# Optimization experiments

Hardware: AMD Instinct MI355X
Metric: run time of the kernel (lower is better)

The kernel has to match this reference:

```python
import jax, jax.numpy as jnp
import numpy as np

B, N, D = 32, 16384, 64        # batch, num inputs (128*128 feature map), slot dim
NS, ITERS, H = 7, 3, 128       # num slots, routing iters, mlp hidden (max(dim,128))
EPS = 1e-8
SCALE = D ** -0.5


def ln(x, g, b):
    # LayerNorm over last dim, eps=1e-5 (matches nn.LayerNorm defaults used)
    m = jnp.mean(x, axis=-1, keepdims=True)
    v = jnp.mean((x - m) ** 2, axis=-1, keepdims=True)
    return (x - m) * jax.lax.rsqrt(v + 1e-5) * g + b


def setup_inputs() -> dict:
    key = jax.random.key(0)
    ks = jax.random.split(key, 24)
    w = lambda k, shape, s=0.02: jax.random.normal(k, shape, dtype=jnp.float32) * s
    inp = {
        "inputs": jax.random.normal(ks[0], (B, N, D), dtype=jnp.float32),
        "noise": jax.random.normal(ks[1], (B, NS, D), dtype=jnp.float32),
        "slots_mu": w(ks[2], (1, 1, D), 1.0),
        "slots_sigma": jnp.abs(w(ks[3], (1, 1, D), 1.0)),  # used directly as std, as in torch.normal(mu, sigma)
        "Wq": w(ks[4], (D, D)), "bq": jnp.zeros((D,), jnp.float32),
        "Wk": w(ks[5], (D, D)), "bk": jnp.zeros((D,), jnp.float32),
        "Wv": w(ks[6], (D, D)), "bv": jnp.zeros((D,), jnp.float32),
        "W_ih": w(ks[7], (3 * D, D)), "W_hh": w(ks[8], (3 * D, D)),
        "b_ih": jnp.zeros((3 * D,), jnp.float32), "b_hh": jnp.zeros((3 * D,), jnp.float32),
        "mW1": w(ks[9], (H, D)), "mb1": jnp.zeros((H,), jnp.float32),
        "mW2": w(ks[10], (D, H)), "mb2": jnp.zeros((D,), jnp.float32),
        "g_in": jnp.ones((D,), jnp.float32), "b_in": jnp.zeros((D,), jnp.float32),
        "g_sl": jnp.ones((D,), jnp.float32), "b_sl": jnp.zeros((D,), jnp.float32),
        "g_ml": jnp.ones((D,), jnp.float32), "b_ml": jnp.zeros((D,), jnp.float32),
    }
    return inp


def reference(inputs, noise, slots_mu, slots_sigma, Wq, bq, Wk, bk, Wv, bv,
              W_ih, W_hh, b_ih, b_hh, mW1, mb1, mW2, mb2,
              g_in, b_in, g_sl, b_sl, g_ml, b_ml):
    # slots ~ Normal(mu, sigma): mu + sigma * eps
    slots = slots_mu + slots_sigma * noise                      # [B, NS, D]
    x = ln(inputs, g_in, b_in)                                  # [B, N, D]
    k = x @ Wk.T + bk                                           # [B, N, D]
    v = x @ Wv.T + bv                                           # [B, N, D]

    for _ in range(ITERS):
        slots_prev = slots
        s = ln(slots, g_sl, b_sl)
        q = s @ Wq.T + bq                                       # [B, NS, D]
        dots = jnp.einsum('bid,bjd->bij', q, k) * SCALE         # [B, NS, N]
        attn = jax.nn.softmax(dots, axis=1) + EPS               # softmax over SLOTS
        attn = attn / jnp.sum(attn, axis=-1, keepdims=True)     # renorm over keys
        updates = jnp.einsum('bjd,bij->bid', v, attn)           # [B, NS, D]
        # GRUCell(updates, slots_prev) over flattened (B*NS, D)
        xg = updates.reshape(-1, D) @ W_ih.T + b_ih             # [B*NS, 3D]
        hg = slots_prev.reshape(-1, D) @ W_hh.T + b_hh
        ir, iz, in_ = jnp.split(xg, 3, axis=-1)
        hr, hz, hn = jnp.split(hg, 3, axis=-1)
        r = jax.nn.sigmoid(ir + hr)
        z = jax.nn.sigmoid(iz + hz)
        n = jnp.tanh(in_ + r * hn)
        h = slots_prev.reshape(-1, D)
        slots = ((1.0 - z) * n + z * h).reshape(B, NS, D)
        # residual MLP
        m = ln(slots, g_ml, b_ml)
        slots = slots + (jax.nn.relu(m @ mW1.T + mb1) @ mW2.T + mb2)
    return slots
```

## Files before the change

### kernel.cpp

```cpp
#include <hip/hip_runtime.h>
#include <hip/hip_bf16.h>

typedef unsigned short u16;
typedef __bf16 bf16x8 __attribute__((ext_vector_type(8)));
typedef float  f32x4  __attribute__((ext_vector_type(4)));

#define N_  16384
#define SCALE_ 0.125f
#define TILE 128
#define TPAD 66
#define APAD 264

__device__ __forceinline__ u16 f2b(float f){
  unsigned u = __float_as_uint(f);
  unsigned r = (u + 0x7fffu + ((u>>16)&1u)) >> 16;
  return (u16)r;
}
__device__ __forceinline__ float blo(unsigned u){ return __uint_as_float(u<<16); }
__device__ __forceinline__ float bhi(unsigned u){ return __uint_as_float(u & 0xffff0000u); }
__device__ __forceinline__ float b2f(u16 v){ return __uint_as_float(((unsigned)v)<<16); }
__device__ __forceinline__ void ld8(const float* __restrict__ p, float* f){
  const float4 a = ((const float4*)p)[0];
  const float4 b = ((const float4*)p)[1];
  f[0]=a.x; f[1]=a.y; f[2]=a.z; f[3]=a.w;
  f[4]=b.x; f[5]=b.y; f[6]=b.z; f[7]=b.w;
}
__device__ __forceinline__ bf16x8 frag8(const float* __restrict__ p){
  float f[8]; ld8(p, f);
  bf16x8 r;
  #pragma unroll
  for (int j=0;j<8;++j) r[j] = (__bf16)f[j];
  return r;
}
__device__ __forceinline__ void unpk4u(uint4 u, float* f){
  f[0]=blo(u.x); f[1]=bhi(u.x);
  f[2]=blo(u.y); f[3]=bhi(u.y);
  f[4]=blo(u.z); f[5]=bhi(u.z);
  f[6]=blo(u.w); f[7]=bhi(u.w);
}

__global__ __launch_bounds__(256) void k_marker(float* __restrict__ out, int n, float val){
  const int i = blockIdx.x*256 + threadIdx.x;
  if (i < n) out[i] = val;
}

__global__ __launch_bounds__(256) void k_init_slots(
  const float* __restrict__ mu, const float* __restrict__ sigma,
  const float* __restrict__ noise, float* __restrict__ slots)
{
  const int idx = blockIdx.x*256 + threadIdx.x;
  const int d = idx & 63;
  slots[idx] = mu[d] + sigma[d] * noise[idx];
}

__global__ __launch_bounds__(256) void k_wkt(const float* __restrict__ Wk, float* __restrict__ wkT){
  const int i = blockIdx.x*256 + threadIdx.x;
  const int e = i>>6, d = i&63;
  wkT[i] = Wk[d*64 + e];
}

__global__ __launch_bounds__(256) void k_xln(
  const float* __restrict__ x, const float* __restrict__ g_in, const float* __restrict__ b_in,
  u16* __restrict__ xout)
{
  const int t = threadIdx.x;
  const long blk = blockIdx.x;
  const float4 gv = *(const float4*)(g_in + (t&15)*4);
  const float4 bb = *(const float4*)(b_in + (t&15)*4);
  const float* xbase = x + blk*16384;
  u16* obase = xout + blk*16384;
  float4 v[16];
  #pragma unroll
  for (int p=0;p<16;++p) v[p] = *(const float4*)(xbase + p*1024 + t*4);
  #pragma unroll
  for (int p=0;p<16;++p){
    float s = v[p].x + v[p].y + v[p].z + v[p].w;
    float q = v[p].x*v[p].x + v[p].y*v[p].y + v[p].z*v[p].z + v[p].w*v[p].w;
    #pragma unroll
    for (int off=1; off<16; off<<=1){ s += __shfl_xor(s, off); q += __shfl_xor(q, off); }
    const float mean = s*(1.f/64.f);
    const float rstd = rsqrtf(q*(1.f/64.f) - mean*mean + 1e-5f);
    const u16 e0 = f2b((v[p].x-mean)*rstd*gv.x + bb.x);
    const u16 e1 = f2b((v[p].y-mean)*rstd*gv.y + bb.y);
    const u16 e2 = f2b((v[p].z-mean)*rstd*gv.z + bb.z);
    const u16 e3 = f2b((v[p].w-mean)*rstd*gv.w + bb.w);
    const unsigned w0 = (unsigned)e0 | ((unsigned)e1<<16);
    const unsigned w1 = (unsigned)e2 | ((unsigned)e3<<16);
    *(uint2*)(obase + p*1024 + t*4) = make_uint2(w0, w1);
  }
}

__global__ __launch_bounds__(256) void k_qln_zero(
  const float* __restrict__ slots, const float* __restrict__ Wq, const float* __restrict__ bq,
  const float* __restrict__ g_sl, const float* __restrict__ b_sl,
  const float* __restrict__ wkT, const float* __restrict__ bk,
  float* __restrict__ qout, float* __restrict__ qkb, float* __restrict__ qbb,
  float* __restrict__ num, float* __restrict__ den, const int do_qk)
{
  const int tid = blockIdx.x*256 + threadIdx.x;
  num[tid] = 0.f;
  if (tid < 224) den[tid] = 0.f;
  const int ri = tid >> 6, lane = tid & 63;
  const float xv = slots[ri*64 + lane];
  float s = xv, ss = xv*xv;
  #pragma unroll
  for (int off=1; off<64; off<<=1){ s += __shfl_xor(s,off); ss += __shfl_xor(ss,off); }
  const float mean = s*(1.f/64.f);
  const float rstd = rsqrtf(ss*(1.f/64.f) - mean*mean + 1e-5f);
  const float sn = (xv-mean)*rstd*g_sl[lane] + b_sl[lane];
  float acc = 0.f;
  for (int d8=0; d8<8; ++d8){
    float wf[8]; ld8(Wq + lane*64 + d8*8, wf);
    #pragma unroll
    for (int j=0;j<8;++j) acc += __shfl(sn, d8*8+j) * wf[j];
  }
  const float qv = acc + bq[lane];
  qout[ri*64+lane] = qv;
  if (do_qk){
    float pb = qv * bk[lane];
    #pragma unroll
    for (int off=1; off<64; off<<=1) pb += __shfl_xor(pb, off);
    if (lane == 0) qbb[ri] = pb;
    float qkv = 0.f;
    for (int d8=0; d8<8; ++d8){
      float wf[8]; ld8(wkT + lane*64 + d8*8, wf);
      #pragma unroll
      for (int j=0;j<8;++j) qkv += __shfl(qv, d8*8+j) * wf[j];
    }
    qkb[ri*64+lane] = qkv;
  }
}

__global__ __launch_bounds__(256) void k_attn3(
  const u16* __restrict__ xln, const float* __restrict__ qkb, const float* __restrict__ qbb,
  float* __restrict__ num, float* __restrict__ den)
{
  __shared__ __align__(16) u16   xs[256*64];
  __shared__ __align__(16) u16   atb[7*APAD];
  __shared__ __align__(16) float qs[448];
  __shared__ float qbs[7];
  __shared__ float den_s[7];
  const int t = threadIdx.x;
  const int b = blockIdx.x >> 5, ch = blockIdx.x & 31;
  for (int i=t;i<448;i+=256) qs[i] = qkb[b*448+i];
  if (t<7){ qbs[t] = qbb[b*7+t]; den_s[t] = 0.f; }
  const int wid = t>>6, lane = t&63;
  const u16* gbase = xln + ((long)b*N_ + ch*512)*64;
  uint4 st[8];
  f32x4 accv = {0.f,0.f,0.f,0.f};

  #pragma unroll
  for (int p=0;p<8;++p) st[p] = *(const uint4*)(gbase + p*2048 + t*8);
  #pragma unroll
  for (int p=0;p<8;++p)
    *(uint4*)&xs[(p*32 + (t>>3))*64 + (((t&7) ^ ((t>>3)&7))<<3)] = st[p];
  __syncthreads();
  #pragma unroll
  for (int p=0;p<8;++p) st[p] = *(const uint4*)(gbase + 16384 + p*2048 + t*8);

  auto phaseA = [&](){
    float acc[7];
    #pragma unroll
    for (int i=0;i<7;++i) acc[i]=0.f;
    #pragma unroll
    for (int seg=0; seg<8; ++seg){
      const uint4 kw = *(const uint4*)&xs[t*64 + ((seg ^ (t&7))<<3)];
      float kf[8]; unpk4u(kw, kf);
      #pragma unroll
      for (int i=0;i<7;++i){
        const float4 qa = *(const float4*)&qs[i*64 + seg*8];
        const float4 qb4 = *(const float4*)&qs[i*64 + seg*8 + 4];
        acc[i] += kf[0]*qa.x + kf[1]*qa.y + kf[2]*qa.z + kf[3]*qa.w
                + kf[4]*qb4.x + kf[5]*qb4.y + kf[6]*qb4.z + kf[7]*qb4.w;
      }
    }
    float mx = -1e30f;
    #pragma unroll
    for (int i=0;i<7;++i){ acc[i] = (acc[i] + qbs[i]) * SCALE_; mx = fmaxf(mx, acc[i]); }
    float e[7]; float sum = 0.f;
    #pragma unroll
    for (int i=0;i<7;++i){ e[i] = __expf(acc[i]-mx); sum += e[i]; }
    const float inv = 1.f/sum;
    float dsum[7];
    #pragma unroll
    for (int i=0;i<7;++i){
      const u16 rb = f2b(e[i]*inv + 1e-8f);
      atb[i*APAD + t] = rb;
      dsum[i] = b2f(rb);
    }
    #pragma unroll
    for (int i=0;i<7;++i){
      #pragma unroll
      for (int off=1; off<64; off<<=1) dsum[i] += __shfl_xor(dsum[i], off);
    }
    if (lane == 0){
      #pragma unroll
      for (int i=0;i<7;++i) atomicAdd(&den_s[i], dsum[i]);
    }
  };

  const int m15 = lane & 15;
  const int kq = (lane>>4)<<3;
  const int dim2 = ((wid<<4) + m15) << 1;
  auto phaseB = [&](){
    #pragma unroll
    for (int ks=0; ks<8; ++ks){
      const int kbase = ks*32 + kq;
      const unsigned a0 = xs[(kbase+0)*64 + ((dim2 ^ (0<<4))>>1)];
      const unsigned a1 = xs[(kbase+1)*64 + ((dim2 ^ (1<<4))>>1)];
      const unsigned a2 = xs[(kbase+2)*64 + ((dim2 ^ (2<<4))>>1)];
      const unsigned a3 = xs[(kbase+3)*64 + ((dim2 ^ (3<<4))>>1)];
      const unsigned a4 = xs[(kbase+4)*64 + ((dim2 ^ (4<<4))>>1)];
      const unsigned a5 = xs[(kbase+5)*64 + ((dim2 ^ (5<<4))>>1)];
      const unsigned a6 = xs[(kbase+6)*64 + ((dim2 ^ (6<<4))>>1)];
      const unsigned a7 = xs[(kbase+7)*64 + ((dim2 ^ (7<<4))>>1)];
      const uint4 aw = make_uint4(a0|(a1<<16), a2|(a3<<16), a4|(a5<<16), a6|(a7<<16));
      const bf16x8 af = __builtin_bit_cast(bf16x8, aw);
      uint4 bw = make_uint4(0u,0u,0u,0u);
      if (m15 < 7) bw = *(const uint4*)&atb[m15*APAD + kbase];
      const bf16x8 bfv = __builtin_bit_cast(bf16x8, bw);
      accv = __builtin_amdgcn_mfma_f32_16x16x32_bf16(af, bfv, accv, 0,0,0);
    }
  };

  phaseA();
  __syncthreads();
  phaseB();
  __syncthreads();
  #pragma unroll
  for (int p=0;p<8;++p)
    *(uint4*)&xs[(p*32 + (t>>3))*64 + (((t&7) ^ ((t>>3)&7))<<3)] = st[p];
  __syncthreads();
  phaseA();
  __syncthreads();
  if (t < 7) atomicAdd(&den[b*7+t], den_s[t]);
  phaseB();

  if (m15 < 7){
    float* np = &num[((long)b*7 + m15)*64 + (wid<<4) + ((lane>>4)<<2)];
    #pragma unroll
    for (int r=0;r<4;++r) atomicAdd(np + r, accv[r]);
  }
}

__global__ __launch_bounds__(256) void k_attn_fused(
  const float* __restrict__ x,
  const float* __restrict__ Wk, const float* __restrict__ bk,
  const float* __restrict__ Wv, const float* __restrict__ bv,
  const float* __restrict__ g_in, const float* __restrict__ b_in,
  const float* __restrict__ qbuf, float* __restrict__ num, float* __restrict__ den)
{
  __shared__ __align__(16) u16   tile[TILE*TPAD];
  __shared__ __align__(16) float qs[7*64];
  __shared__ __align__(16) float at[7*TILE];
  const int t = threadIdx.x;
  const int b = blockIdx.x >> 6, ch = blockIdx.x & 63;
  for (int i=t; i<448; i+=256) qs[i] = qbuf[b*448 + i];
  const int wid = t>>6, lane = t&63;
  const int m = lane & 15, q4 = lane >> 4;
  float gf[16], bfv[16];
  ld8(g_in + q4*8, gf);  ld8(g_in + 32 + q4*8, gf+8);
  ld8(b_in + q4*8, bfv); ld8(b_in + 32 + q4*8, bfv+8);
  const int i0 = wid*2, i1 = wid*2+1;
  float n0=0.f, n1=0.f, d0=0.f, d1=0.f;

  for (int tl=0; tl<2; ++tl){
    const long j0 = (long)ch*256 + tl*TILE;
    const long rowbase = (long)b*N_ + j0 + (long)wid*32;
    __syncthreads();
    bf16x8 af[2][2];
    #pragma unroll
    for (int rg=0; rg<2; ++rg){
      const float* xr = x + (rowbase + rg*16 + m)*64;
      float xf[16];
      ld8(xr + q4*8, xf); ld8(xr + 32 + q4*8, xf+8);
      float s=0.f, ss=0.f;
      #pragma unroll
      for (int i=0;i<16;++i){ s += xf[i]; ss += xf[i]*xf[i]; }
      s  += __shfl_xor(s,16);  s  += __shfl_xor(s,32);
      ss += __shfl_xor(ss,16); ss += __shfl_xor(ss,32);
      const float mean = s*(1.f/64.f);
      const float rstd = rsqrtf(ss*(1.f/64.f) - mean*mean + 1e-5f);
      #pragma unroll
      for (int j=0;j<8;++j){
        af[rg][0][j] = (__bf16)((xf[j]  -mean)*rstd*gf[j]   + bfv[j]);
        af[rg][1][j] = (__bf16)((xf[8+j]-mean)*rstd*gf[8+j] + bfv[8+j]);
      }
    }
    {
      bf16x8 w0[4], w1[4]; float bc[4];
      #pragma unroll
      for (int cg=0; cg<4; ++cg){
        const int n = cg*16 + m;
        w0[cg] = frag8(Wk + n*64 + q4*8);
        w1[cg] = frag8(Wk + n*64 + 32 + q4*8);
        bc[cg] = bk[n];
      }
      #pragma unroll
      for (int rg=0; rg<2; ++rg){
        #pragma unroll
        for (int cg=0; cg<4; ++cg){
          f32x4 acc = {0.f,0.f,0.f,0.f};
          acc = __builtin_amdgcn_mfma_f32_16x16x32_bf16(af[rg][0], w0[cg], acc, 0,0,0);
          acc = __builtin_amdgcn_mfma_f32_16x16x32_bf16(af[rg][1], w1[cg], acc, 0,0,0);
          const int col = cg*16 + m;
          #pragma unroll
          for (int r=0;r<4;++r)
            tile[(wid*32 + rg*16 + q4*4 + r)*TPAD + col] = f2b(acc[r] + bc[cg]);
        }
      }
    }
    __syncthreads();
    if (t < TILE){
      float acc[7];
      #pragma unroll
      for (int i=0;i<7;++i) acc[i]=0.f;
      const unsigned* krow = (const unsigned*)&tile[t*TPAD];
      for (int wq=0; wq<8; ++wq){
        const unsigned k0 = krow[wq*4+0], k1 = krow[wq*4+1], k2 = krow[wq*4+2], k3 = krow[wq*4+3];
        float kf[8];
        kf[0]=blo(k0); kf[1]=bhi(k0); kf[2]=blo(k1); kf[3]=bhi(k1);
        kf[4]=blo(k2); kf[5]=bhi(k2); kf[6]=blo(k3); kf[7]=bhi(k3);
        #pragma unroll
        for (int i=0;i<7;++i){
          const float4 qa = *(const float4*)&qs[i*64 + wq*8];
          const float4 qb = *(const float4*)&qs[i*64 + wq*8 + 4];
          acc[i] += kf[0]*qa.x + kf[1]*qa.y + kf[2]*qa.z + kf[3]*qa.w
                  + kf[4]*qb.x + kf[5]*qb.y + kf[6]*qb.z + kf[7]*qb.w;
        }
      }
      float mx = -1e30f;
      #pragma unroll
      for (int i=0;i<7;++i){ acc[i] *= SCALE_; mx = fmaxf(mx, acc[i]); }
      float e[7]; float sum = 0.f;
      #pragma unroll
      for (int i=0;i<7;++i){ e[i] = __expf(acc[i]-mx); sum += e[i]; }
      const float inv = 1.f/sum;
      #pragma unroll
      for (int i=0;i<7;++i) at[i*TILE + t] = e[i]*inv + 1e-8f;
    }
    __syncthreads();
    {
      bf16x8 w0[4], w1[4]; float bc[4];
      #pragma unroll
      for (int cg=0; cg<4; ++cg){
        const int n = cg*16 + m;
        w0[cg] = frag8(Wv + n*64 + q4*8);
        w1[cg] = frag8(Wv + n*64 + 32 + q4*8);
        bc[cg] = bv[n];
      }
      #pragma unroll
      for (int rg=0; rg<2; ++rg){
        #pragma unroll
        for (int cg=0; cg<4; ++cg){
          f32x4 acc = {0.f,0.f,0.f,0.f};
          acc = __builtin_amdgcn_mfma_f32_16x16x32_bf16(af[rg][0], w0[cg], acc, 0,0,0);
          acc = __builtin_amdgcn_mfma_f32_16x16x32_bf16(af[rg][1], w1[cg], acc, 0,0,0);
          const int col = cg*16 + m;
          #pragma unroll
          for (int r=0;r<4;++r)
            tile[(wid*32 + rg*16 + q4*4 + r)*TPAD + col] = f2b(acc[r] + bc[cg]);
        }
      }
    }
    __syncthreads();
    #pragma unroll 4
    for (int j=0;j<TILE;++j){
      const unsigned vw = ((const unsigned*)&tile[j*TPAD])[lane>>1];
      const float vf = (lane&1) ? bhi(vw) : blo(vw);
      const float a0v = at[i0*TILE+j];
      n0 += a0v*vf; d0 += a0v;
      if (i1 < 7){ const float a1v = at[i1*TILE+j]; n1 += a1v*vf; d1 += a1v; }
    }
  }
  atomicAdd(&num[(b*7+i0)*64 + lane], n0);
  if (lane==0) atomicAdd(&den[b*7+i0], d0);
  if (i1 < 7){
    atomicAdd(&num[(b*7+i1)*64 + lane], n1);
    if (lane==0) atomicAdd(&den[b*7+i1], d1);
  }
}

__global__ __launch_bounds__(256) void k_gru_mlp(
  const float* __restrict__ num, const float* __restrict__ den, float* __restrict__ slots,
  const float* __restrict__ Wv, const float* __restrict__ bv,
  const float* __restrict__ Wih, const float* __restrict__ Whh,
  const float* __restrict__ bih, const float* __restrict__ bhh,
  const float* __restrict__ mW1, const float* __restrict__ mb1,
  const float* __restrict__ mW2, const float* __restrict__ mb2,
  const float* __restrict__ g_ml, const float* __restrict__ b_ml,
  float* __restrict__ outp, const int write_out, const int fastmode)
{
  const int tid = blockIdx.x*256 + threadIdx.x;
  const int ri = tid>>6, lane = tid&63;
  const float dn = den[ri];
  const float a = (dn > 0.f) ? (num[ri*64+lane] / dn) : 0.f;
  float u;
  if (fastmode){
    float acc = 0.f;
    for (int e8=0; e8<8; ++e8){
      float f[8]; ld8(Wv + lane*64 + e8*8, f);
      #pragma unroll
      for (int j=0;j<8;++j) acc += __shfl(a, e8*8+j) * f[j];
    }
    u = acc + bv[lane];
  } else {
    u = a;
  }
  const float h = slots[ri*64+lane];
  float air=0,aiz=0,ain=0,ahr=0,ahz=0,ahn=0;
  for (int d8=0; d8<8; ++d8){
    float fir[8],fiz[8],fin[8],fhr[8],fhz[8],fhn[8];
    ld8(Wih + (      lane)*64 + d8*8, fir);
    ld8(Wih + ( 64 + lane)*64 + d8*8, fiz);
    ld8(Wih + (128 + lane)*64 + d8*8, fin);
    ld8(Whh + (      lane)*64 + d8*8, fhr);
    ld8(Whh + ( 64 + lane)*64 + d8*8, fhz);
    ld8(Whh + (128 + lane)*64 + d8*8, fhn);
    #pragma unroll
    for (int j=0;j<8;++j){
      const float ud = __shfl(u, d8*8+j);
      const float hd = __shfl(h, d8*8+j);
      air += ud*fir[j]; aiz += ud*fiz[j]; ain += ud*fin[j];
      ahr += hd*fhr[j]; ahz += hd*fhz[j]; ahn += hd*fhn[j];
    }
  }
  air += bih[lane]; aiz += bih[64+lane]; ain += bih[128+lane];
  ahr += bhh[lane]; ahz += bhh[64+lane]; ahn += bhh[128+lane];
  const float r = 1.f/(1.f + __expf(-(air+ahr)));
  const float z = 1.f/(1.f + __expf(-(aiz+ahz)));
  const float n = tanhf(ain + r*ahn);
  const float sv = (1.f-z)*n + z*h;
  float s=sv, ss=sv*sv;
  #pragma unroll
  for (int off=1; off<64; off<<=1){ s += __shfl_xor(s,off); ss += __shfl_xor(ss,off); }
  const float mean = s*(1.f/64.f);
  const float rstd = rsqrtf(ss*(1.f/64.f) - mean*mean + 1e-5f);
  const float m = (sv-mean)*rstd*g_ml[lane] + b_ml[lane];
  float h1a=0.f, h1b=0.f;
  for (int d8=0; d8<8; ++d8){
    float f1[8], f2[8];
    ld8(mW1 + (     lane)*64 + d8*8, f1);
    ld8(mW1 + (64 + lane)*64 + d8*8, f2);
    #pragma unroll
    for (int j=0;j<8;++j){
      const float md = __shfl(m, d8*8+j);
      h1a += md*f1[j]; h1b += md*f2[j];
    }
  }
  h1a = fmaxf(h1a + mb1[lane], 0.f);
  h1b = fmaxf(h1b + mb1[64+lane], 0.f);
  float o = 0.f;
  for (int h8=0; h8<8; ++h8){
    float fa[8], fb[8];
    ld8(mW2 + lane*128 + h8*8, fa);
    ld8(mW2 + lane*128 + 64 + h8*8, fb);
    #pragma unroll
    for (int j=0;j<8;++j){
      o += __shfl(h1a, h8*8+j)*fa[j] + __shfl(h1b, h8*8+j)*fb[j];
    }
  }
  o += mb2[lane];
  const float res = sv + o;
  slots[ri*64+lane] = res;
  if (write_out) outp[ri*64+lane] = res;
}

extern "C" void kernel_launch(void* const* d_in, const int* in_sizes, int n_in,
                              void* d_out, int out_size, void* d_ws, size_t ws_size,
                              hipStream_t stream)
{
  float* outp = (float*)d_out;
  static const int EXP[24] = {33554432,14336,64,64, 4096,64, 4096,64, 4096,64,
                              12288,12288,192,192, 8192,128, 8192,64,
                              64,64, 64,64, 64,64};
  if (n_in != 24){ k_marker<<<56,256,0,stream>>>(outp, out_size, 30.f); return; }
  for (int i=0;i<24;++i)
    if (in_sizes[i] != EXP[i]){ k_marker<<<56,256,0,stream>>>(outp, out_size, 40.f+(float)i); return; }
  if (out_size != 14336){ k_marker<<<56,256,0,stream>>>(outp, out_size, 33.f); return; }
  if (ws_size < 200000){ k_marker<<<56,256,0,stream>>>(outp, out_size, 35.f); return; }

  const float* inputs = (const float*)d_in[0];
  const float* noise  = (const float*)d_in[1];
  const float* mu     = (const float*)d_in[2];
  const float* sigma  = (const float*)d_in[3];
  const float* Wq  = (const float*)d_in[4];  const float* bq  = (const float*)d_in[5];
  const float* Wk  = (const float*)d_in[6];  const float* bk  = (const float*)d_in[7];
  const float* Wv  = (const float*)d_in[8];  const float* bv  = (const float*)d_in[9];
  const float* Wih = (const float*)d_in[10]; const float* Whh = (const float*)d_in[11];
  const float* bih = (const float*)d_in[12]; const float* bhh = (const float*)d_in[13];
  const float* mW1 = (const float*)d_in[14]; const float* mb1 = (const float*)d_in[15];
  const float* mW2 = (const float*)d_in[16]; const float* mb2 = (const float*)d_in[17];
  const float* g_in = (const float*)d_in[18]; const float* b_in = (const float*)d_in[19];
  const float* g_sl = (const float*)d_in[20]; const float* b_sl = (const float*)d_in[21];
  const float* g_ml = (const float*)d_in[22]; const float* b_ml = (const float*)d_in[23];

  char* ws = (char*)d_ws;
  float* slots = (float*)ws;
  float* qbuf  = (float*)(ws + 57344);
  float* qkb   = (float*)(ws + 114688);
  float* num   = (float*)(ws + 172032);
  float* den   = (float*)(ws + 229376);
  float* qbb   = (float*)(ws + 230272);
  float* wkT   = (float*)(ws + 231168);
  u16* xln     = (u16*)(ws + 247808);
  const bool fast = (ws_size >= (size_t)247808 + 67108864ull);

  k_init_slots<<<56,256,0,stream>>>(mu, sigma, noise, slots);
  if (fast){
    k_wkt<<<16,256,0,stream>>>(Wk, wkT);
    k_xln<<<2048,256,0,stream>>>(inputs, g_in, b_in, xln);
  }
  for (int it=0; it<3; ++it){
    k_qln_zero<<<56,256,0,stream>>>(slots, Wq, bq, g_sl, b_sl, wkT, bk,
                                    qbuf, qkb, qbb, num, den, fast ? 1 : 0);
    if (fast)
      k_attn3<<<1024,256,0,stream>>>(xln, qkb, qbb, num, den);
    else
      k_attn_fused<<<2048,256,0,stream>>>(inputs, Wk, bk, Wv, bv, g_in, b_in, qbuf, num, den);
    k_gru_mlp<<<56,256,0,stream>>>(num, den, slots, Wv, bv, Wih, Whh, bih, bhh,
                                   mW1, mb1, mW2, mb2, g_ml, b_ml,
                                   outp, it==2 ? 1 : 0, fast ? 1 : 0);
  }
}
```

Measured before the change: 452.8 us.

## Use MFMA for slot-key dots, shrink attention tiles, fuse q projection into GRU kernel

The attention kernel now computes the q·k logits with bf16 MFMA instructions instead of scalar FMAs. It processes 128 keys per block across 4096 blocks, replacing 512-key blocks that double-buffered through registers. The q/LayerNorm projection and the num/den zeroing move into the init and GRU/MLP kernels, which removes one launch per iteration. In exchange, q is rounded to bf16 and there are more global atomics on den and num, since the block-local den reduction is gone and there are four times as many blocks.

```diff
diff --git a/kernel.cpp b/kernel.cpp
--- a/kernel.cpp
+++ b/kernel.cpp
@@ -9,7 +9,7 @@
 #define SCALE_ 0.125f
 #define TILE 128
 #define TPAD 66
-#define APAD 264
+#define AP4 136
 
 __device__ __forceinline__ u16 f2b(float f){
   unsigned u = __float_as_uint(f);
@@ -32,25 +32,65 @@
   for (int j=0;j<8;++j) r[j] = (__bf16)f[j];
   return r;
 }
-__device__ __forceinline__ void unpk4u(uint4 u, float* f){
-  f[0]=blo(u.x); f[1]=bhi(u.x);
-  f[2]=blo(u.y); f[3]=bhi(u.y);
-  f[4]=blo(u.z); f[5]=bhi(u.z);
-  f[6]=blo(u.w); f[7]=bhi(u.w);
-}
 
 __global__ __launch_bounds__(256) void k_marker(float* __restrict__ out, int n, float val){
   const int i = blockIdx.x*256 + threadIdx.x;
   if (i < n) out[i] = val;
 }
 
-__global__ __launch_bounds__(256) void k_init_slots(
+__device__ __forceinline__ void q_from_slots(
+  const float sv, const int ri, const int lane,
+  const float* __restrict__ Wq, const float* __restrict__ bq,
+  const float* __restrict__ g_sl, const float* __restrict__ b_sl,
+  const float* __restrict__ wkT, const float* __restrict__ bk,
+  float* __restrict__ qout, float* __restrict__ qkb, float* __restrict__ qbb,
+  const int do_qk)
+{
+  float s = sv, ss = sv*sv;
+  #pragma unroll
+  for (int off=1; off<64; off<<=1){ s += __shfl_xor(s,off); ss += __shfl_xor(ss,off); }
+  const float mean = s*(1.f/64.f);
+  const float rstd = rsqrtf(ss*(1.f/64.f) - mean*mean + 1e-5f);
+  const float sn = (sv-mean)*rstd*g_sl[lane] + b_sl[lane];
+  float acc = 0.f;
+  for (int d8=0; d8<8; ++d8){
+    float wf[8]; ld8(Wq + lane*64 + d8*8, wf);
+    #pragma unroll
+    for (int j=0;j<8;++j) acc += __shfl(sn, d8*8+j) * wf[j];
+  }
+  const float qv = acc + bq[lane];
+  qout[ri*64+lane] = qv;
+  if (do_qk){
+    float pb = qv * bk[lane];
+    #pragma unroll
+    for (int off=1; off<64; off<<=1) pb += __shfl_xor(pb, off);
+    if (lane == 0) qbb[ri] = pb;
+    float qkv = 0.f;
+    for (int d8=0; d8<8; ++d8){
+      float wf[8]; ld8(wkT + lane*64 + d8*8, wf);
+      #pragma unroll
+      for (int j=0;j<8;++j) qkv += __shfl(qv, d8*8+j) * wf[j];
+    }
+    qkb[ri*64+lane] = qkv;
+  }
+}
+
+__global__ __launch_bounds__(256) void k_init_slots_q(
   const float* __restrict__ mu, const float* __restrict__ sigma,
-  const float* __restrict__ noise, float* __restrict__ slots)
-{
-  const int idx = blockIdx.x*256 + threadIdx.x;
-  const int d = idx & 63;
-  slots[idx] = mu[d] + sigma[d] * noise[idx];
+  const float* __restrict__ noise, float* __restrict__ slots,
+  const float* __restrict__ Wq, const float* __restrict__ bq,
+  const float* __restrict__ g_sl, const float* __restrict__ b_sl,
+  const float* __restrict__ wkT, const float* __restrict__ bk,
+  float* __restrict__ qout, float* __restrict__ qkb, float* __restrict__ qbb,
+  float* __restrict__ num, float* __restrict__ den, const int do_qk)
+{
+  const int tid = blockIdx.x*256 + threadIdx.x;
+  const int ri = tid>>6, lane = tid&63;
+  const float sv = mu[lane] + sigma[lane] * noise[tid];
+  slots[tid] = sv;
+  num[tid] = 0.f;
+  if (tid < 224) den[tid] = 0.f;
+  q_from_slots(sv, ri, lane, Wq, bq, g_sl, b_sl, wkT, bk, qout, qkb, qbb, do_qk);
 }
 
 __global__ __launch_bounds__(256) void k_wkt(const float* __restrict__ Wk, float* __restrict__ wkT){
@@ -90,93 +130,67 @@
   }
 }
 
-__global__ __launch_bounds__(256) void k_qln_zero(
-  const float* __restrict__ slots, const float* __restrict__ Wq, const float* __restrict__ bq,
-  const float* __restrict__ g_sl, const float* __restrict__ b_sl,
-  const float* __restrict__ wkT, const float* __restrict__ bk,
-  float* __restrict__ qout, float* __restrict__ qkb, float* __restrict__ qbb,
-  float* __restrict__ num, float* __restrict__ den, const int do_qk)
-{
-  const int tid = blockIdx.x*256 + threadIdx.x;
-  num[tid] = 0.f;
-  if (tid < 224) den[tid] = 0.f;
-  const int ri = tid >> 6, lane = tid & 63;
-  const float xv = slots[ri*64 + lane];
-  float s = xv, ss = xv*xv;
-  #pragma unroll
-  for (int off=1; off<64; off<<=1){ s += __shfl_xor(s,off); ss += __shfl_xor(ss,off); }
-  const float mean = s*(1.f/64.f);
-  const float rstd = rsqrtf(ss*(1.f/64.f) - mean*mean + 1e-5f);
-  const float sn = (xv-mean)*rstd*g_sl[lane] + b_sl[lane];
-  float acc = 0.f;
-  for (int d8=0; d8<8; ++d8){
-    float wf[8]; ld8(Wq + lane*64 + d8*8, wf);
-    #pragma unroll
-    for (int j=0;j<8;++j) acc += __shfl(sn, d8*8+j) * wf[j];
-  }
-  const float qv = acc + bq[lane];
-  qout[ri*64+lane] = qv;
-  if (do_qk){
-    float pb = qv * bk[lane];
-    #pragma unroll
-    for (int off=1; off<64; off<<=1) pb += __shfl_xor(pb, off);
-    if (lane == 0) qbb[ri] = pb;
-    float qkv = 0.f;
-    for (int d8=0; d8<8; ++d8){
-      float wf[8]; ld8(wkT + lane*64 + d8*8, wf);
-      #pragma unroll
-      for (int j=0;j<8;++j) qkv += __shfl(qv, d8*8+j) * wf[j];
-    }
-    qkb[ri*64+lane] = qkv;
-  }
-}
-
-__global__ __launch_bounds__(256) void k_attn3(
+__global__ __launch_bounds__(256) void k_attn4(
   const u16* __restrict__ xln, const float* __restrict__ qkb, const float* __restrict__ qbb,
   float* __restrict__ num, float* __restrict__ den)
 {
-  __shared__ __align__(16) u16   xs[256*64];
-  __shared__ __align__(16) u16   atb[7*APAD];
-  __shared__ __align__(16) float qs[448];
+  __shared__ __align__(16) u16   xs[128*64];
+  __shared__ __align__(16) u16   atb[7*AP4];
+  __shared__ __align__(16) float dlds[128*9];
   __shared__ float qbs[7];
-  __shared__ float den_s[7];
   const int t = threadIdx.x;
-  const int b = blockIdx.x >> 5, ch = blockIdx.x & 31;
-  for (int i=t;i<448;i+=256) qs[i] = qkb[b*448+i];
-  if (t<7){ qbs[t] = qbb[b*7+t]; den_s[t] = 0.f; }
+  const int b = blockIdx.x >> 7, ch = blockIdx.x & 127;
   const int wid = t>>6, lane = t&63;
-  const u16* gbase = xln + ((long)b*N_ + ch*512)*64;
-  uint4 st[8];
-  f32x4 accv = {0.f,0.f,0.f,0.f};
-
-  #pragma unroll
-  for (int p=0;p<8;++p) st[p] = *(const uint4*)(gbase + p*2048 + t*8);
-  #pragma unroll
-  for (int p=0;p<8;++p)
+  const int m15 = lane&15, g4 = lane>>4;
+
+  const u16* gbase = xln + ((long)b*N_ + ch*128)*64;
+  uint4 st[4];
+  #pragma unroll
+  for (int p=0;p<4;++p) st[p] = *(const uint4*)(gbase + p*2048 + t*8);
+  if (t < 7) qbs[t] = qbb[b*7+t];
+  bf16x8 qf[2];
+  #pragma unroll
+  for (int f=0; f<2; ++f){
+    float tmp[8];
+    if (m15 < 7){ ld8(qkb + b*448 + m15*64 + f*32 + g4*8, tmp); }
+    else {
+      #pragma unroll
+      for (int j=0;j<8;++j) tmp[j]=0.f;
+    }
+    #pragma unroll
+    for (int j=0;j<8;++j) qf[f][j] = (__bf16)tmp[j];
+  }
+  #pragma unroll
+  for (int p=0;p<4;++p)
     *(uint4*)&xs[(p*32 + (t>>3))*64 + (((t&7) ^ ((t>>3)&7))<<3)] = st[p];
   __syncthreads();
-  #pragma unroll
-  for (int p=0;p<8;++p) st[p] = *(const uint4*)(gbase + 16384 + p*2048 + t*8);
-
-  auto phaseA = [&](){
+
+  #pragma unroll
+  for (int mt=0; mt<2; ++mt){
+    const int kr = (wid<<5) + (mt<<4) + m15;
+    f32x4 dacc = {0.f,0.f,0.f,0.f};
+    #pragma unroll
+    for (int f=0; f<2; ++f){
+      const int c = (f<<2) + g4;
+      const uint4 aw = *(const uint4*)&xs[kr*64 + ((c ^ (kr&7))<<3)];
+      dacc = __builtin_amdgcn_mfma_f32_16x16x32_bf16(
+               __builtin_bit_cast(bf16x8, aw), qf[f], dacc, 0,0,0);
+    }
+    if (m15 < 7){
+      const int krow = (wid<<5) + (mt<<4) + (g4<<2);
+      #pragma unroll
+      for (int r=0;r<4;++r) dlds[(krow+r)*9 + m15] = dacc[r];
+    }
+  }
+  __syncthreads();
+
+  if (t < 128){
     float acc[7];
     #pragma unroll
-    for (int i=0;i<7;++i) acc[i]=0.f;
-    #pragma unroll
-    for (int seg=0; seg<8; ++seg){
-      const uint4 kw = *(const uint4*)&xs[t*64 + ((seg ^ (t&7))<<3)];
-      float kf[8]; unpk4u(kw, kf);
-      #pragma unroll
-      for (int i=0;i<7;++i){
-        const float4 qa = *(const float4*)&qs[i*64 + seg*8];
-        const float4 qb4 = *(const float4*)&qs[i*64 + seg*8 + 4];
-        acc[i] += kf[0]*qa.x + kf[1]*qa.y + kf[2]*qa.z + kf[3]*qa.w
-                + kf[4]*qb4.x + kf[5]*qb4.y + kf[6]*qb4.z + kf[7]*qb4.w;
-      }
-    }
+    for (int i=0;i<7;++i) acc[i] = (dlds[t*9+i] + qbs[i]) * SCALE_;
     float mx = -1e30f;
     #pragma unroll
-    for (int i=0;i<7;++i){ acc[i] = (acc[i] + qbs[i]) * SCALE_; mx = fmaxf(mx, acc[i]); }
+    for (int i=0;i<7;++i) mx = fmaxf(mx, acc[i]);
     float e[7]; float sum = 0.f;
     #pragma unroll
     for (int i=0;i<7;++i){ e[i] = __expf(acc[i]-mx); sum += e[i]; }
@@ -185,7 +199,7 @@
     #pragma unroll
     for (int i=0;i<7;++i){
       const u16 rb = f2b(e[i]*inv + 1e-8f);
-      atb[i*APAD + t] = rb;
+      atb[i*AP4 + t] = rb;
       dsum[i] = b2f(rb);
     }
     #pragma unroll
@@ -195,49 +209,33 @@
     }
     if (lane == 0){
       #pragma unroll
-      for (int i=0;i<7;++i) atomicAdd(&den_s[i], dsum[i]);
-    }
-  };
-
-  const int m15 = lane & 15;
-  const int kq = (lane>>4)<<3;
+      for (int i=0;i<7;++i) atomicAdd(&den[b*7+i], dsum[i]);
+    }
+  }
+  __syncthreads();
+
   const int dim2 = ((wid<<4) + m15) << 1;
-  auto phaseB = [&](){
-    #pragma unroll
-    for (int ks=0; ks<8; ++ks){
-      const int kbase = ks*32 + kq;
-      const unsigned a0 = xs[(kbase+0)*64 + ((dim2 ^ (0<<4))>>1)];
-      const unsigned a1 = xs[(kbase+1)*64 + ((dim2 ^ (1<<4))>>1)];
-      const unsigned a2 = xs[(kbase+2)*64 + ((dim2 ^ (2<<4))>>1)];
-      const unsigned a3 = xs[(kbase+3)*64 + ((dim2 ^ (3<<4))>>1)];
-      const unsigned a4 = xs[(kbase+4)*64 + ((dim2 ^ (4<<4))>>1)];
-      const unsigned a5 = xs[(kbase+5)*64 + ((dim2 ^ (5<<4))>>1)];
-      const unsigned a6 = xs[(kbase+6)*64 + ((dim2 ^ (6<<4))>>1)];
-      const unsigned a7 = xs[(kbase+7)*64 + ((dim2 ^ (7<<4))>>1)];
-      const uint4 aw = make_uint4(a0|(a1<<16), a2|(a3<<16), a4|(a5<<16), a6|(a7<<16));
-      const bf16x8 af = __builtin_bit_cast(bf16x8, aw);
-      uint4 bw = make_uint4(0u,0u,0u,0u);
-      if (m15 < 7) bw = *(const uint4*)&atb[m15*APAD + kbase];
-      const bf16x8 bfv = __builtin_bit_cast(bf16x8, bw);
-      accv = __builtin_amdgcn_mfma_f32_16x16x32_bf16(af, bfv, accv, 0,0,0);
-    }
-  };
-
-  phaseA();
-  __syncthreads();
-  phaseB();
-  __syncthreads();
-  #pragma unroll
-  for (int p=0;p<8;++p)
-    *(uint4*)&xs[(p*32 + (t>>3))*64 + (((t&7) ^ ((t>>3)&7))<<3)] = st[p];
-  __syncthreads();
-  phaseA();
-  __syncthreads();
-  if (t < 7) atomicAdd(&den[b*7+t], den_s[t]);
-  phaseB();
-
+  f32x4 accv = {0.f,0.f,0.f,0.f};
+  #pragma unroll
+  for (int ks=0; ks<4; ++ks){
+    const int kbase = (ks<<5) + (g4<<3);
+    const unsigned a0 = xs[(kbase+0)*64 + ((dim2 ^ (0<<4))>>1)];
+    const unsigned a1 = xs[(kbase+1)*64 + ((dim2 ^ (1<<4))>>1)];
+    const unsigned a2 = xs[(kbase+2)*64 + ((dim2 ^ (2<<4))>>1)];
+    const unsigned a3 = xs[(kbase+3)*64 + ((dim2 ^ (3<<4))>>1)];
+    const unsigned a4 = xs[(kbase+4)*64 + ((dim2 ^ (4<<4))>>1)];
+    const unsigned a5 = xs[(kbase+5)*64 + ((dim2 ^ (5<<4))>>1)];
+    const unsigned a6 = xs[(kbase+6)*64 + ((dim2 ^ (6<<4))>>1)];
+    const unsigned a7 = xs[(kbase+7)*64 + ((dim2 ^ (7<<4))>>1)];
+    const uint4 aw = make_uint4(a0|(a1<<16), a2|(a3<<16), a4|(a5<<16), a6|(a7<<16));
+    const bf16x8 af = __builtin_bit_cast(bf16x8, aw);
+    uint4 bw = make_uint4(0u,0u,0u,0u);
+    if (m15 < 7) bw = *(const uint4*)&atb[m15*AP4 + kbase];
+    const bf16x8 bfv = __builtin_bit_cast(bf16x8, bw);
+    accv = __builtin_amdgcn_mfma_f32_16x16x32_bf16(af, bfv, accv, 0,0,0);
+  }
   if (m15 < 7){
-    float* np = &num[((long)b*7 + m15)*64 + (wid<<4) + ((lane>>4)<<2)];
+    float* np = &num[((long)b*7 + m15)*64 + (wid<<4) + (g4<<2)];
     #pragma unroll
     for (int r=0;r<4;++r) atomicAdd(np + r, accv[r]);
   }
@@ -382,19 +380,26 @@
 }
 
 __global__ __launch_bounds__(256) void k_gru_mlp(
-  const float* __restrict__ num, const float* __restrict__ den, float* __restrict__ slots,
+  float* __restrict__ num, float* __restrict__ den, float* __restrict__ slots,
   const float* __restrict__ Wv, const float* __restrict__ bv,
   const float* __restrict__ Wih, const float* __restrict__ Whh,
   const float* __restrict__ bih, const float* __restrict__ bhh,
   const float* __restrict__ mW1, const float* __restrict__ mb1,
   const float* __restrict__ mW2, const float* __restrict__ mb2,
   const float* __restrict__ g_ml, const float* __restrict__ b_ml,
-  float* __restrict__ outp, const int write_out, const int fastmode)
+  const float* __restrict__ Wq, const float* __restrict__ bq,
+  const float* __restrict__ g_sl, const float* __restrict__ b_sl,
+  const float* __restrict__ wkT, const float* __restrict__ bk,
+  float* __restrict__ qout, float* __restrict__ qkb, float* __restrict__ qbb,
+  float* __restrict__ outp,
+  const int write_out, const int fastmode, const int do_q, const int do_qk)
 {
   const int tid = blockIdx.x*256 + threadIdx.x;
   const int ri = tid>>6, lane = tid&63;
   const float dn = den[ri];
-  const float a = (dn > 0.f) ? (num[ri*64+lane] / dn) : 0.f;
+  const float a = (dn > 0.f) ? (num[tid] / dn) : 0.f;
+  num[tid] = 0.f;
+  if (lane == 0) den[ri] = 0.f;
   float u;
   if (fastmode){
     float acc = 0.f;
@@ -407,7 +412,7 @@
   } else {
     u = a;
   }
-  const float h = slots[ri*64+lane];
+  const float h = slots[tid];
   float air=0,aiz=0,ain=0,ahr=0,ahz=0,ahn=0;
   for (int d8=0; d8<8; ++d8){
     float fir[8],fiz[8],fin[8],fhr[8],fhz[8],fhn[8];
@@ -462,8 +467,10 @@
   }
   o += mb2[lane];
   const float res = sv + o;
-  slots[ri*64+lane] = res;
-  if (write_out) outp[ri*64+lane] = res;
+  slots[tid] = res;
+  if (write_out) outp[tid] = res;
+  if (do_q)
+    q_from_slots(res, ri, lane, Wq, bq, g_sl, b_sl, wkT, bk, qout, qkb, qbb, do_qk);
 }
 
 extern "C" void kernel_launch(void* const* d_in, const int* in_sizes, int n_in,
@@ -478,7 +485,7 @@
   for (int i=0;i<24;++i)
     if (in_sizes[i] != EXP[i]){ k_marker<<<56,256,0,stream>>>(outp, out_size, 40.f+(float)i); return; }
   if (out_size != 14336){ k_marker<<<56,256,0,stream>>>(outp, out_size, 33.f); return; }
-  if (ws_size < 200000){ k_marker<<<56,256,0,stream>>>(outp, out_size, 35.f); return; }
+  if (ws_size < 300000){ k_marker<<<56,256,0,stream>>>(outp, out_size, 35.f); return; }
 
   const float* inputs = (const float*)d_in[0];
   const float* noise  = (const float*)d_in[1];
@@ -506,20 +513,23 @@
   u16* xln     = (u16*)(ws + 247808);
   const bool fast = (ws_size >= (size_t)247808 + 67108864ull);
 
-  k_init_slots<<<56,256,0,stream>>>(mu, sigma, noise, slots);
   if (fast){
     k_wkt<<<16,256,0,stream>>>(Wk, wkT);
     k_xln<<<2048,256,0,stream>>>(inputs, g_in, b_in, xln);
   }
+  k_init_slots_q<<<56,256,0,stream>>>(mu, sigma, noise, slots,
+                                      Wq, bq, g_sl, b_sl, wkT, bk,
+                                      qbuf, qkb, qbb, num, den, fast ? 1 : 0);
   for (int it=0; it<3; ++it){
-    k_qln_zero<<<56,256,0,stream>>>(slots, Wq, bq, g_sl, b_sl, wkT, bk,
-                                    qbuf, qkb, qbb, num, den, fast ? 1 : 0);
     if (fast)
-      k_attn3<<<1024,256,0,stream>>>(xln, qkb, qbb, num, den);
+      k_attn4<<<4096,256,0,stream>>>(xln, qkb, qbb, num, den);
     else
       k_attn_fused<<<2048,256,0,stream>>>(inputs, Wk, bk, Wv, bv, g_in, b_in, qbuf, num, den);
     k_gru_mlp<<<56,256,0,stream>>>(num, den, slots, Wv, bv, Wih, Whh, bih, bhh,
                                    mW1, mb1, mW2, mb2, g_ml, b_ml,
-                                   outp, it==2 ? 1 : 0, fast ? 1 : 0);
-  }
-}
+                                   Wq, bq, g_sl, b_sl, wkT, bk,
+                                   qbuf, qkb, qbb, outp,
+                                   it==2 ? 1 : 0, fast ? 1 : 0,
+                                   it<2 ? 1 : 0, (fast && it<2) ? 1 : 0);
+  }
+}
```

After: 889.2 us. +96.4%, slower.
